# Kernel tuning notes

Measured on AMD Instinct MI355X. Metric: run time of the kernel, lower is better.

## Reference

```python
import jax, jax.numpy as jnp
import numpy as np

CHANNELS = 512
COND_DIM = 768
NUM_HEADS = 8
NUM_GROUPS = 32
EPS = 1e-5


def setup_inputs() -> dict:
    key = jax.random.key(0)
    ks = jax.random.split(key, 8)
    B, H, W, C, S = 8, 64, 64, CHANNELS, 256
    x = jax.random.normal(ks[0], (B, H, W, C), dtype=jnp.float32)
    cond_tokens = jax.random.normal(ks[1], (B, S, COND_DIM), dtype=jnp.float32)
    gn_scale = jnp.ones((C,), dtype=jnp.float32)
    gn_bias = jnp.zeros((C,), dtype=jnp.float32)
    Wq = jax.random.normal(ks[2], (C, CHANNELS), dtype=jnp.float32) * 0.02
    Wk = jax.random.normal(ks[3], (COND_DIM, CHANNELS), dtype=jnp.float32) * 0.02
    Wv = jax.random.normal(ks[4], (COND_DIM, CHANNELS), dtype=jnp.float32) * 0.02
    Wo = jax.random.normal(ks[5], (CHANNELS, CHANNELS), dtype=jnp.float32) * 0.02
    bo = jnp.zeros((CHANNELS,), dtype=jnp.float32)
    return {"x": x, "cond_tokens": cond_tokens, "gn_scale": gn_scale,
            "gn_bias": gn_bias, "Wq": Wq, "Wk": Wk, "Wv": Wv, "Wo": Wo, "bo": bo}


def group_norm(x, scale, bias):
    # x: (B,H,W,C); normalize over H,W and channels within each of NUM_GROUPS groups
    b, h, w, c = x.shape
    xg = x.reshape(b, h, w, NUM_GROUPS, c // NUM_GROUPS)
    mean = jnp.mean(xg, axis=(1, 2, 4), keepdims=True)
    var = jnp.var(xg, axis=(1, 2, 4), keepdims=True)
    xn = (xg - mean) * jax.lax.rsqrt(var + EPS)
    return xn.reshape(b, h, w, c) * scale + bias


def reference(x, cond_tokens, gn_scale, gn_bias, Wq, Wk, Wv, Wo, bo):
    b, h, w, c = x.shape
    head_dim = CHANNELS // NUM_HEADS
    x_seq = group_norm(x, gn_scale, gn_bias).reshape(b, h * w, c)
    # projections
    q = (x_seq @ Wq).reshape(b, -1, NUM_HEADS, head_dim).transpose(0, 2, 1, 3)
    k = (cond_tokens @ Wk).reshape(b, -1, NUM_HEADS, head_dim).transpose(0, 2, 1, 3)
    v = (cond_tokens @ Wv).reshape(b, -1, NUM_HEADS, head_dim).transpose(0, 2, 1, 3)
    scores = jnp.einsum('bhqd,bhkd->bhqk', q, k) / np.sqrt(head_dim).astype(np.float32)
    attn = jax.nn.softmax(scores, axis=-1)
    out = jnp.einsum('bhqk,bhkd->bhqd', attn, v)
    out = out.transpose(0, 2, 1, 3).reshape(b, h * w, CHANNELS)
    out = out @ Wo + bo
    return x + out.reshape(b, h, w, c)
```

## Files before the change

### kernel.cpp

```cpp
#include <hip/hip_runtime.h>
#include <hip/hip_bf16.h>

typedef unsigned short u16;
typedef unsigned int u32;
typedef __attribute__((ext_vector_type(8))) __bf16 bf16x8;
typedef __attribute__((ext_vector_type(4))) float f32x4;
typedef __attribute__((ext_vector_type(16))) float f32x16;
typedef __attribute__((ext_vector_type(4))) u32 u32x4;

#define SCL 0.18033688011112042f

#define DEVFN static __device__ __forceinline__

DEVFN float bf2f(u16 v) { union { u32 u; float f; } x; x.u = (u32)v << 16; return x.f; }
DEVFN u16 f2bf(float f) {
    union { float f; u32 u; } x; x.f = f;
    u32 r = x.u + 0x7fff + ((x.u >> 16) & 1);
    return (u16)(r >> 16);
}

union BF2 { struct { __bf16 lo, hi; } s; u32 w; };
DEVFN u32 pk2(float a, float b) { BF2 t; t.s.lo = (__bf16)a; t.s.hi = (__bf16)b; return t.w; }

DEVFN void gload_lds16(const u16* g, u16* l) {
    __builtin_amdgcn_global_load_lds((const __attribute__((address_space(1))) u32*)g,
                                     (__attribute__((address_space(3))) u32*)l, 16, 0, 0);
}

template<int OUTMODE, bool BIAS, bool RES, bool PERB, bool RESBF>
__global__ __launch_bounds__(256)
void gemm_bt(const u16* __restrict__ A, const u16* __restrict__ B,
             const u16* __restrict__ B2,
             void* __restrict__ Cv, void* __restrict__ Cv2,
             const float* __restrict__ bias, const void* __restrict__ res,
             int K, int lda, int ldb, int ldc, float scale)
{
    __shared__ u16 smem[16384];
    const int tid = threadIdx.x;
    const int lane = tid & 63, wave = tid >> 6;
    const int wr = wave >> 1, wc = wave & 1;
    const u16* Bsel = (OUTMODE == 3 && blockIdx.z) ? B2 : B;
    if constexpr (PERB) Bsel += (long)(blockIdx.x >> 5) * 262144;
    const u16* Bb = Bsel + (long)blockIdx.y * 128 * ldb;
    const u16* Ab = A + (long)blockIdx.x * 128 * lda;
    const int ra = tid >> 2, ca = (tid & 3) * 8;
    const int foff = ((lane & 15) * 4 + (lane >> 4)) * 8;

    f32x4 acc[4][4];
#pragma unroll
    for (int i = 0; i < 4; ++i)
#pragma unroll
        for (int j = 0; j < 4; ++j) acc[i][j] = (f32x4){0.f, 0.f, 0.f, 0.f};

    const int nt = K >> 5;
    auto stage = [&](int t, u16* buf) {
#pragma unroll
        for (int p = 0; p < 2; ++p)
            gload_lds16(Ab + (long)(p * 64 + ra) * lda + t * 32 + ca,
                        buf + (p * 256 + tid) * 8);
#pragma unroll
        for (int p = 0; p < 2; ++p)
            gload_lds16(Bb + (long)(p * 64 + ra) * ldb + t * 32 + ca,
                        buf + 4096 + (p * 256 + tid) * 8);
    };

    stage(0, smem);
    int cur = 0;
    for (int t = 0; t < nt; ++t) {
        asm volatile("s_waitcnt vmcnt(0)" ::: "memory");
        __syncthreads();
        const int nxt = cur ^ 1;
        u16* cA = smem + cur * 8192;
        u16* cB = smem + cur * 8192 + 4096;
        if (t + 1 < nt) stage(t + 1, smem + nxt * 8192);
        bf16x8 av[4], bv[4];
#pragma unroll
        for (int i = 0; i < 4; ++i) av[i] = *(const bf16x8*)(cA + (wr * 4 + i) * 512 + foff);
#pragma unroll
        for (int j = 0; j < 4; ++j) bv[j] = *(const bf16x8*)(cB + (wc * 4 + j) * 512 + foff);
        __builtin_amdgcn_s_setprio(1);
#pragma unroll
        for (int i = 0; i < 4; ++i)
#pragma unroll
            for (int j = 0; j < 4; ++j)
                acc[i][j] = __builtin_amdgcn_mfma_f32_16x16x32_bf16(av[i], bv[j], acc[i][j], 0, 0, 0);
        __builtin_amdgcn_s_setprio(0);
        cur = nxt;
    }

    const int m0 = blockIdx.x * 128 + wr * 64 + (lane >> 4) * 4;
    const int n0 = blockIdx.y * 128 + wc * 64 + (lane & 15);
    if constexpr (OUTMODE == 0) {
        u16* Cb = (u16*)Cv;
        const float* bp = bias;
        if constexpr (PERB && BIAS) bp += (blockIdx.x >> 5) * 512;
#pragma unroll
        for (int i = 0; i < 4; ++i)
#pragma unroll
            for (int j = 0; j < 4; ++j) {
                int n = n0 + j * 16;
                float bv_ = BIAS ? bp[n] : 0.f;
#pragma unroll
                for (int r = 0; r < 4; ++r) {
                    int m = m0 + i * 16 + r;
                    Cb[(long)m * ldc + n] = f2bf(acc[i][j][r] * scale + bv_);
                }
            }
    } else if constexpr (OUTMODE == 1) {
        float* cl = (float*)smem;
        float* Co = (float*)Cv;
#pragma unroll
        for (int i = 0; i < 4; ++i) {
            __syncthreads();
#pragma unroll
            for (int j = 0; j < 4; ++j)
#pragma unroll
                for (int r = 0; r < 4; ++r) {
                    int rl = wr * 16 + (lane >> 4) * 4 + r;
                    int col = wc * 64 + j * 16 + (lane & 15);
                    cl[rl * 132 + col] = acc[i][j][r];
                }
            __syncthreads();
            int rl = tid >> 3;
            int c0 = (tid & 7) * 16;
            long m = (long)blockIdx.x * 128 + i * 16 + (rl & 15) + (rl >> 4) * 64;
            long n = (long)blockIdx.y * 128 + c0;
#pragma unroll
            for (int q = 0; q < 4; ++q) {
                float4 v = *(float4*)(cl + rl * 132 + c0 + q * 4);
                float4 o;
                o.x = v.x * scale; o.y = v.y * scale;
                o.z = v.z * scale; o.w = v.w * scale;
                if constexpr (BIAS) {
                    float4 b4 = *(const float4*)(bias + n + q * 4);
                    o.x += b4.x; o.y += b4.y; o.z += b4.z; o.w += b4.w;
                }
                if constexpr (RES) {
                    if constexpr (RESBF) {
                        ushort4 r4 = *(const ushort4*)((const u16*)res + m * ldc + n + q * 4);
                        o.x += bf2f(r4.x); o.y += bf2f(r4.y);
                        o.z += bf2f(r4.z); o.w += bf2f(r4.w);
                    } else {
                        float4 r4 = *(const float4*)((const float*)res + m * ldc + n + q * 4);
                        o.x += r4.x; o.y += r4.y; o.z += r4.z; o.w += r4.w;
                    }
                }
                *(float4*)(Co + m * ldc + n + q * 4) = o;
            }
        }
    } else {
        if (blockIdx.z == 0) {
            u16* Cb = (u16*)Cv;
#pragma unroll
            for (int i = 0; i < 4; ++i)
#pragma unroll
                for (int j = 0; j < 4; ++j) {
                    int n = n0 + j * 16;
#pragma unroll
                    for (int r = 0; r < 4; ++r) {
                        int m = m0 + i * 16 + r;
                        Cb[(long)m * ldc + n] = f2bf(acc[i][j][r] * scale);
                    }
                }
        } else {
#pragma unroll
            for (int i = 0; i < 4; ++i) {
                int m = m0 + i * 16;
                int b = m >> 8, s = m & 255;
#pragma unroll
                for (int j = 0; j < 4; ++j) {
                    int n = n0 + j * 16;
                    int h = n >> 6, d = n & 63;
                    ushort4 pk;
                    pk.x = f2bf(acc[i][j][0]); pk.y = f2bf(acc[i][j][1]);
                    pk.z = f2bf(acc[i][j][2]); pk.w = f2bf(acc[i][j][3]);
                    *(ushort4*)((u16*)Cv2 + (((long)(b * 8 + h) * 64 + d) * 256 + s)) = pk;
                }
            }
        }
    }
}

union U8 { u32 w[4]; bf16x8 v; };

__global__ __launch_bounds__(512, 4)
void attn_fused(const u16* __restrict__ Q, const u16* __restrict__ K,
                const u16* __restrict__ Vt, u16* __restrict__ O)
{
    __shared__ u16 lds[40960];
    const int tid = threadIdx.x, lane = tid & 63, wave = tid >> 6;
    const int bh = blockIdx.y, b = bh >> 3, h = bh & 7;
    const int l31 = lane & 31, lh = lane >> 5;
    const long q0 = (long)b * 4096 + blockIdx.x * 256 + wave * 32;
    const bool hiHalf = (lh != 0);

    {
        const u16* Kb_ = K + (long)b * 256 * 512 + h * 64;
        const u16* Vb_ = Vt + (long)bh * 16384;
#pragma unroll
        for (int it = 0; it < 4; ++it) {
            int f = it * 8 + wave;
            int st = f >> 2, kc = f & 3;
            gload_lds16(Kb_ + (long)(st * 32 + l31) * 512 + kc * 16 + lh * 8,
                        lds + f * 512 + lane * 8);
            int dt = f >> 4, ks = f & 15;
            gload_lds16(Vb_ + (long)(dt * 32 + l31) * 256 + ks * 16 + lh * 8,
                        lds + 16384 + f * 512 + lane * 8);
        }
    }
    bf16x8 qf[4];
    {
        const u16* Qp = Q + (q0 + l31) * 512 + h * 64 + lh * 8;
#pragma unroll
        for (int kc = 0; kc < 4; ++kc) qf[kc] = *(const bf16x8*)(Qp + kc * 16);
    }
    asm volatile("s_waitcnt vmcnt(0)" ::: "memory");
    __syncthreads();

    f32x16 oacc[2];
#pragma unroll
    for (int dt = 0; dt < 2; ++dt)
#pragma unroll
        for (int r = 0; r < 16; ++r) oacc[dt][r] = 0.f;
    float m_run = -3e38f, sum_run = 0.f;

#pragma unroll
    for (int st = 0; st < 8; ++st) {
        f32x16 sc;
#pragma unroll
        for (int r = 0; r < 16; ++r) sc[r] = 0.f;
        __builtin_amdgcn_s_setprio(1);
#pragma unroll
        for (int kc = 0; kc < 4; ++kc) {
            bf16x8 af = *(const bf16x8*)(lds + (st * 4 + kc) * 512 + lane * 8);
            sc = __builtin_amdgcn_mfma_f32_32x32x16_bf16(af, qf[kc], sc, 0, 0, 0);
        }
        __builtin_amdgcn_s_setprio(0);
        float tm = sc[0];
#pragma unroll
        for (int r = 1; r < 16; ++r) tm = fmaxf(tm, sc[r]);
        tm = fmaxf(tm, __shfl_xor(tm, 32));
        if (!__all(tm <= m_run + 8.f)) {
            float mnew = fmaxf(m_run, tm);
            float fac = exp2f(m_run - mnew);
            m_run = mnew;
            sum_run *= fac;
#pragma unroll
            for (int dt = 0; dt < 2; ++dt)
#pragma unroll
                for (int r = 0; r < 16; ++r) oacc[dt][r] *= fac;
        }
#pragma unroll
        for (int r = 0; r < 16; ++r) {
            float e = exp2f(sc[r] - m_run);
            sc[r] = e; sum_run += e;
        }
        u32 c[8], x[8];
#pragma unroll
        for (int i = 0; i < 8; ++i) c[i] = pk2(sc[2 * i], sc[2 * i + 1]);
#pragma unroll
        for (int i = 0; i < 8; ++i) x[i] = (u32)__shfl_xor((int)c[i], 32);
        U8 p0, p1;
        p0.w[0] = hiHalf ? x[2] : c[0];  p0.w[1] = hiHalf ? x[3] : c[1];
        p0.w[2] = hiHalf ? c[2] : x[0];  p0.w[3] = hiHalf ? c[3] : x[1];
        p1.w[0] = hiHalf ? x[6] : c[4];  p1.w[1] = hiHalf ? x[7] : c[5];
        p1.w[2] = hiHalf ? c[6] : x[4];  p1.w[3] = hiHalf ? c[7] : x[5];
        __builtin_amdgcn_s_setprio(1);
#pragma unroll
        for (int dt = 0; dt < 2; ++dt) {
            bf16x8 v0 = *(const bf16x8*)(lds + 16384 + (dt * 16 + st * 2) * 512 + lane * 8);
            bf16x8 v1 = *(const bf16x8*)(lds + 16384 + (dt * 16 + st * 2 + 1) * 512 + lane * 8);
            oacc[dt] = __builtin_amdgcn_mfma_f32_32x32x16_bf16(v0, p0.v, oacc[dt], 0, 0, 0);
            oacc[dt] = __builtin_amdgcn_mfma_f32_32x32x16_bf16(v1, p1.v, oacc[dt], 0, 0, 0);
        }
        __builtin_amdgcn_s_setprio(0);
    }

    sum_run += __shfl_xor(sum_run, 32);
    float inv = 1.f / sum_run;

    u16* ow = lds + 32768 + (wave & 3) * 2048;
    const int shift = wave >> 2;
#pragma unroll
    for (int s_ = 0; s_ < 2; ++s_) {
        if (s_ == 1) __syncthreads();
        if (shift == s_) {
            const int q = l31;
#pragma unroll
            for (int dt = 0; dt < 2; ++dt)
#pragma unroll
                for (int rq = 0; rq < 4; ++rq) {
                    int d = dt * 32 + rq * 8 + 4 * lh;
                    u32 w0 = pk2(oacc[dt][rq * 4 + 0] * inv, oacc[dt][rq * 4 + 1] * inv);
                    u32 w1 = pk2(oacc[dt][rq * 4 + 2] * inv, oacc[dt][rq * 4 + 3] * inv);
                    int byte = q * 128 + ((d * 2) ^ ((q & 7) << 4));
                    *(u32*)((char*)ow + byte) = w0;
                    *(u32*)((char*)ow + byte + 4) = w1;
                }
#pragma unroll
            for (int i = 0; i < 4; ++i) {
                int qq = (lane >> 3) + i * 8;
                int byte = qq * 128 + (((lane & 7) * 16) ^ ((qq & 7) << 4));
                bf16x8 val = *(const bf16x8*)((char*)ow + byte);
                *(bf16x8*)(O + (q0 + qq) * 512 + h * 64 + (lane & 7) * 8) = val;
            }
        }
    }
}

__global__ __launch_bounds__(256)
void gn_part(const float* __restrict__ x, float* __restrict__ part,
             u16* __restrict__ xb)
{
    const int b = blockIdx.x, ch = blockIdx.y;
    const long base = ((long)b * 4096 + ch * 64) * 512;
    const float* bx = x + base;
    u16* bo = xb + base;
    const int t = threadIdx.x;
    const int c4 = t & 127, r0 = t >> 7;
    float sum = 0.f, sq = 0.f;
    for (int rr = r0; rr < 64; rr += 2) {
        float4 v = *(const float4*)(bx + (long)rr * 512 + c4 * 4);
        sum += v.x + v.y + v.z + v.w;
        sq  += v.x * v.x + v.y * v.y + v.z * v.z + v.w * v.w;
        uint2 w;
        w.x = pk2(v.x, v.y); w.y = pk2(v.z, v.w);
        *(uint2*)(bo + (long)rr * 512 + c4 * 4) = w;
    }
    __shared__ float s0[128], s1[128];
    if (t >= 128) { s0[c4] = sum; s1[c4] = sq; }
    __syncthreads();
    if (t < 128) {
        sum += s0[c4]; sq += s1[c4];
        sum += __shfl_down(sum, 2); sum += __shfl_down(sum, 1);
        sq  += __shfl_down(sq, 2);  sq  += __shfl_down(sq, 1);
        if ((t & 3) == 0) {
            int g = t >> 2;
            float* pp = part + (long)(b * 64 + ch) * 64;
            pp[g] = sum; pp[32 + g] = sq;
        }
    }
}

__global__ __launch_bounds__(256)
void gn_coef(const float* __restrict__ part, const float* __restrict__ gscale,
             const float* __restrict__ gbias, float* __restrict__ coefA,
             float* __restrict__ coefD)
{
    const int t = threadIdx.x;
    const int b = t >> 5, g = t & 31;
    float S = 0.f, Q = 0.f;
    for (int ch = 0; ch < 64; ++ch) {
        const float* pp = part + (long)(b * 64 + ch) * 64;
        S += pp[g]; Q += pp[32 + g];
    }
    float mean = S * (1.f / 65536.f);
    float var = Q * (1.f / 65536.f) - mean * mean;
    float rstd = rsqrtf(var + 1e-5f);
#pragma unroll
    for (int cc = 0; cc < 16; ++cc) {
        int c = g * 16 + cc;
        float a = gscale[c] * rstd;
        coefA[b * 512 + c] = a;
        coefD[b * 512 + c] = gbias[c] - mean * a;
    }
}

__global__ __launch_bounds__(256)
void scale_wq(const float* __restrict__ Wq, const float* __restrict__ cfA,
              u16* __restrict__ WqS)
{
    __shared__ u16 t[32][33];
    const int b = blockIdx.z;
    const int r0 = blockIdx.y * 32, c0 = blockIdx.x * 32;
    int tx = threadIdx.x & 31, ty = threadIdx.x >> 5;
    for (int i = ty; i < 32; i += 8)
        t[i][tx] = f2bf(Wq[(long)(r0 + i) * 512 + c0 + tx] * cfA[b * 512 + r0 + i] * SCL);
    __syncthreads();
    for (int i = ty; i < 32; i += 8)
        WqS[(long)b * 262144 + (long)(c0 + i) * 512 + r0 + tx] = t[tx][i];
}

__global__ __launch_bounds__(256)
void dq_bias(const float* __restrict__ Wq, const float* __restrict__ cfD,
             float* __restrict__ dq)
{
    const int b = blockIdx.x, t = threadIdx.x;
    float a0 = 0.f, a1 = 0.f;
    for (int c = 0; c < 512; ++c) {
        float d = cfD[b * 512 + c];
        a0 += d * Wq[(long)c * 512 + t];
        a1 += d * Wq[(long)c * 512 + t + 256];
    }
    dq[b * 512 + t] = a0 * SCL;
    dq[b * 512 + t + 256] = a1 * SCL;
}

__global__ __launch_bounds__(256)
void conv_bf16(const float* __restrict__ in, u16* __restrict__ out)
{
    long e = ((long)blockIdx.x * 256 + threadIdx.x) * 8;
    float4 v0 = *(const float4*)(in + e);
    float4 v1 = *(const float4*)(in + e + 4);
    float f[8] = { v0.x, v0.y, v0.z, v0.w, v1.x, v1.y, v1.z, v1.w };
    u32x4 o;
#pragma unroll
    for (int q = 0; q < 4; ++q)
        o[q] = (u32)f2bf(f[q * 2]) | ((u32)f2bf(f[q * 2 + 1]) << 16);
    *(u32x4*)(out + e) = o;
}

__global__ __launch_bounds__(256)
void transpose_all(const float* __restrict__ Wk, const float* __restrict__ Wv,
                   const float* __restrict__ Wo,
                   u16* __restrict__ WkT, u16* __restrict__ WvT,
                   u16* __restrict__ WoT)
{
    __shared__ u16 t[32][33];
    const int z = blockIdx.z;
    const float* in = (z == 0) ? Wk : (z == 1) ? Wv : Wo;
    u16* out = (z == 0) ? WkT : (z == 1) ? WvT : WoT;
    const int R = (z < 2) ? 768 : 512, C = 512;
    const int r0 = blockIdx.y * 32, c0 = blockIdx.x * 32;
    if (r0 >= R) return;
    int tx = threadIdx.x & 31, ty = threadIdx.x >> 5;
    for (int i = ty; i < 32; i += 8) t[i][tx] = f2bf(in[(long)(r0 + i) * C + c0 + tx]);
    __syncthreads();
    for (int i = ty; i < 32; i += 8) out[(long)(c0 + i) * R + r0 + tx] = t[tx][i];
}

extern "C" void kernel_launch(void* const* d_in, const int* in_sizes, int n_in,
                              void* d_out, int out_size, void* d_ws, size_t ws_size,
                              hipStream_t stream)
{
    const float* x    = (const float*)d_in[0];
    const float* cond = (const float*)d_in[1];
    const float* gsc  = (const float*)d_in[2];
    const float* gbi  = (const float*)d_in[3];
    const float* Wq   = (const float*)d_in[4];
    const float* Wk   = (const float*)d_in[5];
    const float* Wv   = (const float*)d_in[6];
    const float* Wo   = (const float*)d_in[7];
    const float* bo   = (const float*)d_in[8];

    char* ws = (char*)d_ws;
    size_t off = 0;
    auto alloc = [&](size_t bytes) -> void* {
        void* p = ws + off; off += (bytes + 255) & ~(size_t)255; return p;
    };
    u16* WkT    = (u16*)alloc(512 * 768 * 2);
    u16* WvT    = (u16*)alloc(512 * 768 * 2);
    u16* WoT    = (u16*)alloc(512 * 512 * 2);
    u16* WqS    = (u16*)alloc(8l * 512 * 512 * 2);
    float* cfA  = (float*)alloc(8 * 512 * 4);
    float* cfD  = (float*)alloc(8 * 512 * 4);
    float* dq   = (float*)alloc(8 * 512 * 4);
    float* part = (float*)alloc(8 * 64 * 64 * 4);
    u16* condb  = (u16*)alloc(2048l * 768 * 2);
    u16* xb     = (u16*)alloc(33554432);
    u16* Ob     = (u16*)alloc(33554432);
    u16* Qb     = (u16*)alloc(33554432);
    u16* Kb     = (u16*)alloc(2048l * 512 * 2);
    u16* Vt     = (u16*)alloc(2097152);

    transpose_all<<<dim3(16, 24, 3), 256, 0, stream>>>(Wk, Wv, Wo, WkT, WvT, WoT);
    conv_bf16<<<768, 256, 0, stream>>>(cond, condb);

    gn_part<<<dim3(8, 64), 256, 0, stream>>>(x, part, xb);
    gn_coef<<<1, 256, 0, stream>>>(part, gsc, gbi, cfA, cfD);
    scale_wq<<<dim3(16, 16, 8), 256, 0, stream>>>(Wq, cfA, WqS);
    dq_bias<<<8, 256, 0, stream>>>(Wq, cfD, dq);

    gemm_bt<3, false, false, false, false><<<dim3(16, 4, 2), 256, 0, stream>>>(
        condb, WkT, WvT, Kb, Vt, nullptr, nullptr, 768, 768, 768, 512, 1.f);

    gemm_bt<0, true, false, true, false><<<dim3(256, 4), 256, 0, stream>>>(
        xb, WqS, nullptr, Qb, nullptr, dq, nullptr, 512, 512, 512, 512, 1.f);

    attn_fused<<<dim3(16, 64), 512, 0, stream>>>(Qb, Kb, Vt, Ob);

    gemm_bt<1, true, true, false, true><<<dim3(256, 4), 256, 0, stream>>>(
        Ob, WoT, nullptr, d_out, nullptr, bo, xb, 512, 512, 512, 512, 1.f);
}
```

Before: 197.4 us.

## Triple-buffer GEMM LDS pipeline, remap staging layout, parallelize dq_bias

New measurement: 218.7 us. 1.11x slower.

```diff
diff --git a/kernel.cpp b/kernel.cpp
--- a/kernel.cpp
+++ b/kernel.cpp
@@ -35,7 +35,7 @@
              const float* __restrict__ bias, const void* __restrict__ res,
              int K, int lda, int ldb, int ldc, float scale)
 {
-    __shared__ u16 smem[16384];
+    __shared__ u16 smem[24576];
     const int tid = threadIdx.x;
     const int lane = tid & 63, wave = tid >> 6;
     const int wr = wave >> 1, wc = wave & 1;
@@ -43,8 +43,8 @@
     if constexpr (PERB) Bsel += (long)(blockIdx.x >> 5) * 262144;
     const u16* Bb = Bsel + (long)blockIdx.y * 128 * ldb;
     const u16* Ab = A + (long)blockIdx.x * 128 * lda;
-    const int ra = tid >> 2, ca = (tid & 3) * 8;
-    const int foff = ((lane & 15) * 4 + (lane >> 4)) * 8;
+    const int sr = (tid >> 6) * 16 + (tid & 15);
+    const int sc2 = ((tid >> 4) & 3) * 8;
 
     f32x4 acc[4][4];
 #pragma unroll
@@ -56,28 +56,31 @@
     auto stage = [&](int t, u16* buf) {
 #pragma unroll
         for (int p = 0; p < 2; ++p)
-            gload_lds16(Ab + (long)(p * 64 + ra) * lda + t * 32 + ca,
+            gload_lds16(Ab + (long)(p * 64 + sr) * lda + t * 32 + sc2,
                         buf + (p * 256 + tid) * 8);
 #pragma unroll
         for (int p = 0; p < 2; ++p)
-            gload_lds16(Bb + (long)(p * 64 + ra) * ldb + t * 32 + ca,
+            gload_lds16(Bb + (long)(p * 64 + sr) * ldb + t * 32 + sc2,
                         buf + 4096 + (p * 256 + tid) * 8);
     };
 
     stage(0, smem);
+    stage(1, smem + 8192);
     int cur = 0;
     for (int t = 0; t < nt; ++t) {
-        asm volatile("s_waitcnt vmcnt(0)" ::: "memory");
-        __syncthreads();
-        const int nxt = cur ^ 1;
+        if (t + 1 < nt) asm volatile("s_waitcnt vmcnt(4)" ::: "memory");
+        else            asm volatile("s_waitcnt vmcnt(0)" ::: "memory");
+        __builtin_amdgcn_s_barrier();
+        asm volatile("" ::: "memory");
         u16* cA = smem + cur * 8192;
-        u16* cB = smem + cur * 8192 + 4096;
-        if (t + 1 < nt) stage(t + 1, smem + nxt * 8192);
+        u16* cB = cA + 4096;
+        int nx2 = cur + 2; if (nx2 >= 3) nx2 -= 3;
+        if (t + 2 < nt) stage(t + 2, smem + nx2 * 8192);
         bf16x8 av[4], bv[4];
 #pragma unroll
-        for (int i = 0; i < 4; ++i) av[i] = *(const bf16x8*)(cA + (wr * 4 + i) * 512 + foff);
-#pragma unroll
-        for (int j = 0; j < 4; ++j) bv[j] = *(const bf16x8*)(cB + (wc * 4 + j) * 512 + foff);
+        for (int i = 0; i < 4; ++i) av[i] = *(const bf16x8*)(cA + (wr * 4 + i) * 512 + lane * 8);
+#pragma unroll
+        for (int j = 0; j < 4; ++j) bv[j] = *(const bf16x8*)(cB + (wc * 4 + j) * 512 + lane * 8);
         __builtin_amdgcn_s_setprio(1);
 #pragma unroll
         for (int i = 0; i < 4; ++i)
@@ -85,7 +88,7 @@
             for (int j = 0; j < 4; ++j)
                 acc[i][j] = __builtin_amdgcn_mfma_f32_16x16x32_bf16(av[i], bv[j], acc[i][j], 0, 0, 0);
         __builtin_amdgcn_s_setprio(0);
-        cur = nxt;
+        cur = (cur + 1 == 3) ? 0 : cur + 1;
     }
 
     const int m0 = blockIdx.x * 128 + wr * 64 + (lane >> 4) * 4;
@@ -385,15 +388,20 @@
 void dq_bias(const float* __restrict__ Wq, const float* __restrict__ cfD,
              float* __restrict__ dq)
 {
-    const int b = blockIdx.x, t = threadIdx.x;
-    float a0 = 0.f, a1 = 0.f;
-    for (int c = 0; c < 512; ++c) {
-        float d = cfD[b * 512 + c];
-        a0 += d * Wq[(long)c * 512 + t];
-        a1 += d * Wq[(long)c * 512 + t + 256];
-    }
-    dq[b * 512 + t] = a0 * SCL;
-    dq[b * 512 + t + 256] = a1 * SCL;
+    const int b = blockIdx.x, nc = blockIdx.y;
+    const int t = threadIdx.x;
+    const int n = nc * 64 + (t & 63);
+    const int cq = t >> 6;
+    float a = 0.f;
+    for (int c = cq * 128; c < cq * 128 + 128; ++c)
+        a += cfD[b * 512 + c] * Wq[(long)c * 512 + n];
+    __shared__ float red[256];
+    red[t] = a;
+    __syncthreads();
+    if (t < 64) {
+        float s = red[t] + red[64 + t] + red[128 + t] + red[192 + t];
+        dq[b * 512 + nc * 64 + t] = s * SCL;
+    }
 }
 
 __global__ __launch_bounds__(256)
@@ -469,7 +477,7 @@
     gn_part<<<dim3(8, 64), 256, 0, stream>>>(x, part, xb);
     gn_coef<<<1, 256, 0, stream>>>(part, gsc, gbi, cfA, cfD);
     scale_wq<<<dim3(16, 16, 8), 256, 0, stream>>>(Wq, cfA, WqS);
-    dq_bias<<<8, 256, 0, stream>>>(Wq, cfD, dq);
+    dq_bias<<<dim3(8, 8), 256, 0, stream>>>(Wq, cfD, dq);
 
     gemm_bt<3, false, false, false, false><<<dim3(16, 4, 2), 256, 0, stream>>>(
         condb, WkT, WvT, Kb, Vt, nullptr, nullptr, 768, 768, 768, 512, 1.f);
```
